# Kernel optimization log

Measured on AMD Instinct MI355X. Metric: run time of the kernel, lower is better.

Reference implementation:

```python
import jax, jax.numpy as jnp
import numpy as np

B, S, D_IN, D_QK, D_V = 4, 4096, 1024, 64, 64

def setup_inputs() -> dict:
    key = jax.random.key(0)
    ks = jax.random.split(key, 8)
    sd = 1.0 / np.sqrt(D_IN)
    return {
        "X": jax.random.normal(ks[0], (B, S, D_IN), dtype=jnp.float32),
        "mask": jnp.ones((B, S, 1), dtype=jnp.float32),
        "Wq": jax.random.uniform(ks[1], (D_IN, D_QK), jnp.float32, -sd, sd),
        "bq": jax.random.uniform(ks[2], (D_QK,), jnp.float32, -sd, sd),
        "Wk": jax.random.uniform(ks[3], (D_IN, D_QK), jnp.float32, -sd, sd),
        "bk": jax.random.uniform(ks[4], (D_QK,), jnp.float32, -sd, sd),
        "Wv": jax.random.uniform(ks[5], (D_IN, D_V), jnp.float32, -sd, sd),
        "bv": jax.random.uniform(ks[6], (D_V,), jnp.float32, -sd, sd),
    }

def reference(X, mask, Wq, bq, Wk, bk, Wv, bv):
    # ReLU-activated projections (no head split, no 1/sqrt(d) scaling)
    q = jax.nn.relu(jnp.einsum('bsd,df->bsf', X, Wq) + bq)   # [B,S,D_QK]
    k = jax.nn.relu(jnp.einsum('bsd,df->bsf', X, Wk) + bk)   # [B,S,D_QK]
    v = jax.nn.relu(jnp.einsum('bsd,df->bsf', X, Wv) + bv)   # [B,S,D_V]
    scores = jax.nn.softmax(jnp.einsum('bqf,bkf->bqk', q, k), axis=-1)  # [B,S,S]
    return jnp.einsum('bqk,bkf->bqf', scores, v) * mask       # mask applied AFTER AV
```

## Files before the change

kernel.cpp:

```cpp
#include <hip/hip_runtime.h>


typedef short s16x8 __attribute__((ext_vector_type(8)));
typedef float fx4   __attribute__((ext_vector_type(4)));
typedef unsigned short u16x4 __attribute__((ext_vector_type(4)));

#define LOG2E 1.4426950408889634f

__device__ __forceinline__ unsigned short f2bf(float x) {
    unsigned int u = __float_as_uint(x);
    u += 0x7FFFu + ((u >> 16) & 1u);
    return (unsigned short)(u >> 16);
}
__device__ __forceinline__ float bf2f(unsigned short b) {
    return __uint_as_float(((unsigned int)b) << 16);
}

__global__ __launch_bounds__(256) void prep_w_kernel(
    const float* __restrict__ Wq, const float* __restrict__ Wk, const float* __restrict__ Wv,
    unsigned short* __restrict__ wt_hi, unsigned short* __restrict__ wt_lo)
{
    __shared__ __align__(16) unsigned short sh[64][72];
    __shared__ __align__(16) unsigned short sl[64][72];

    const int y  = blockIdx.x;
    const int kt = blockIdx.y;
    const float* W = (y == 0) ? Wq : (y == 1) ? Wk : Wv;
    const int t  = threadIdx.x;

    const int kl = t >> 2;
    const int c0 = (t & 3) * 16;
    const float* src = W + (size_t)(kt * 64 + kl) * 64 + c0;
    #pragma unroll
    for (int j = 0; j < 4; j++) {
        fx4 v = *(const fx4*)(src + j * 4);
        #pragma unroll
        for (int i = 0; i < 4; i++) {
            float x = v[i];
            unsigned short h = f2bf(x);
            unsigned short l = f2bf(x - bf2f(h));
            sh[c0 + j * 4 + i][kl] = h;
            sl[c0 + j * 4 + i][kl] = l;
        }
    }
    __syncthreads();

    const int c  = t >> 2;
    const int k0 = (t & 3) * 16;
    size_t o = (size_t)(y * 64 + c) * 1024 + kt * 64 + k0;
    *(s16x8*)(wt_hi + o)     = *(const s16x8*)&sh[c][k0];
    *(s16x8*)(wt_hi + o + 8) = *(const s16x8*)&sh[c][k0 + 8];
    *(s16x8*)(wt_lo + o)     = *(const s16x8*)&sl[c][k0];
    *(s16x8*)(wt_lo + o + 8) = *(const s16x8*)&sl[c][k0 + 8];
}

__global__ __launch_bounds__(512, 4) void proj_kernel(
    const float* __restrict__ X,
    const unsigned short* __restrict__ wt_hi, const unsigned short* __restrict__ wt_lo,
    const float* __restrict__ bq, const float* __restrict__ bk, const float* __restrict__ bv,
    unsigned short* __restrict__ q_hi, unsigned short* __restrict__ q_lo,
    unsigned short* __restrict__ k_bf, unsigned short* __restrict__ vt_g)
{
    __shared__ __align__(16) unsigned short a_buf[2][64][72];
    __shared__ __align__(16) unsigned short b_hi[64][72];
    __shared__ __align__(16) unsigned short b_lo[64][72];

    const int tid  = threadIdx.x;
    const int lane = tid & 63;
    const int w    = tid >> 6;
    const int quad = lane >> 4;
    const int l15  = lane & 15;
    const int rs   = w & 3;
    const int ch   = w >> 2;

    const int f   = blockIdx.x;
    const int xcd = f & 7;
    const int jj  = f >> 3;
    const int y   = jj % 3;
    const int m0  = ((jj / 3) * 8 + xcd) * 64;

    fx4 acc[2];
    acc[0] = (fx4){0.f, 0.f, 0.f, 0.f};
    acc[1] = (fx4){0.f, 0.f, 0.f, 0.f};

    const int xrow = tid >> 4;
    const int xoff = (tid & 15) * 4;
    const int wrow = tid >> 3;
    const int woff = (tid & 7) * 8;

    const float* xb0 = X + (size_t)(m0 + xrow) * 1024 + xoff;
    const float* xb1 = X + (size_t)(m0 + xrow + 32) * 1024 + xoff;
    const size_t wb  = (size_t)(y * 64 + wrow) * 1024 + woff;

    fx4   xr[4][2];
    s16x8 wrh[2], wrl[2];
    #pragma unroll
    for (int d = 0; d < 4; d++) {
        xr[d][0] = *(const fx4*)(xb0 + d * 64);
        xr[d][1] = *(const fx4*)(xb1 + d * 64);
    }
    #pragma unroll
    for (int d = 0; d < 2; d++) {
        wrh[d] = *(const s16x8*)(wt_hi + wb + d * 64);
        wrl[d] = *(const s16x8*)(wt_lo + wb + d * 64);
    }

    #pragma unroll 4
    for (int kc = 0; kc < 16; kc++) {
        if (kc) __syncthreads();
        #pragma unroll
        for (int i = 0; i < 2; i++) {
            fx4 xv = xr[kc & 3][i];
            unsigned short h0 = f2bf(xv.x), h1 = f2bf(xv.y), h2 = f2bf(xv.z), h3 = f2bf(xv.w);
            unsigned short l0 = f2bf(xv.x - bf2f(h0)), l1 = f2bf(xv.y - bf2f(h1));
            unsigned short l2 = f2bf(xv.z - bf2f(h2)), l3 = f2bf(xv.w - bf2f(h3));
            *(u16x4*)&a_buf[0][xrow + i * 32][xoff] = (u16x4){h0, h1, h2, h3};
            *(u16x4*)&a_buf[1][xrow + i * 32][xoff] = (u16x4){l0, l1, l2, l3};
        }
        *(s16x8*)&b_hi[wrow][woff] = wrh[kc & 1];
        *(s16x8*)&b_lo[wrow][woff] = wrl[kc & 1];
        __syncthreads();

        if (kc < 12) {
            xr[kc & 3][0] = *(const fx4*)(xb0 + (kc + 4) * 64);
            xr[kc & 3][1] = *(const fx4*)(xb1 + (kc + 4) * 64);
        }
        if (kc < 14) {
            wrh[kc & 1] = *(const s16x8*)(wt_hi + wb + (kc + 2) * 64);
            wrl[kc & 1] = *(const s16x8*)(wt_lo + wb + (kc + 2) * 64);
        }

        s16x8 ah[2], al[2];
        #pragma unroll
        for (int ks = 0; ks < 2; ks++) {
            int r = rs * 16 + l15;
            ah[ks] = *(const s16x8*)&a_buf[0][r][ks * 32 + quad * 8];
            al[ks] = *(const s16x8*)&a_buf[1][r][ks * 32 + quad * 8];
        }
        #pragma unroll
        for (int nt = 0; nt < 2; nt++) {
            #pragma unroll
            for (int ks = 0; ks < 2; ks++) {
                s16x8 bh = *(const s16x8*)&b_hi[ch * 32 + nt * 16 + l15][ks * 32 + quad * 8];
                s16x8 bl = *(const s16x8*)&b_lo[ch * 32 + nt * 16 + l15][ks * 32 + quad * 8];
                acc[nt] = __builtin_amdgcn_mfma_f32_16x16x32_bf16(ah[ks], bh, acc[nt], 0, 0, 0);
                acc[nt] = __builtin_amdgcn_mfma_f32_16x16x32_bf16(ah[ks], bl, acc[nt], 0, 0, 0);
                acc[nt] = __builtin_amdgcn_mfma_f32_16x16x32_bf16(al[ks], bh, acc[nt], 0, 0, 0);
            }
        }
    }
    __syncthreads();

    const float* bias = (y == 0) ? bq : (y == 1) ? bk : bv;
    const int b   = m0 >> 12;
    const int s0b = m0 & 4095;
    unsigned short* vtr = &a_buf[0][0][0];

    #pragma unroll
    for (int nt = 0; nt < 2; nt++) {
        int col = ch * 32 + nt * 16 + l15;
        float bb = bias[col];
        int rloc = rs * 16 + quad * 4;
        #pragma unroll
        for (int r = 0; r < 4; r++) {
            float v = acc[nt][r] + bb;
            v = fmaxf(v, 0.f);
            size_t grow = (size_t)(m0 + rloc + r);
            if (y == 0) {
                unsigned short h = f2bf(v);
                unsigned short l = f2bf(v - bf2f(h));
                q_hi[grow * 64 + col] = h;
                q_lo[grow * 64 + col] = l;
            } else if (y == 1) {
                k_bf[grow * 64 + col] = f2bf(v);
            } else {
                vtr[col * 72 + rloc + r] = f2bf(v);
            }
        }
    }
    if (y == 2) {
        __syncthreads();
        int row = tid >> 3;
        int off = (tid & 7) * 8;
        s16x8 vv = *(const s16x8*)&vtr[row * 72 + off];
        *(s16x8*)(vt_g + (size_t)(b * 64 + row) * 4096 + s0b + off) = vv;
    }
}

__global__ __launch_bounds__(256, 6) void attn_kernel(
    const unsigned short* __restrict__ q_hi, const unsigned short* __restrict__ q_lo,
    const unsigned short* __restrict__ k_bf, const unsigned short* __restrict__ vt_g,
    unsigned short* __restrict__ pOb, float* __restrict__ pL)
{
    __shared__ __align__(16) unsigned short kt[64][72];
    __shared__ __align__(16) unsigned short vt[64][72];
    __shared__ __align__(16) unsigned short pt[4][16][40];

    const int tid  = threadIdx.x;
    const int lane = tid & 63;
    const int w    = tid >> 6;
    const int quad = lane >> 4;
    const int l15  = lane & 15;
    const int ck   = blockIdx.y;
    const int b    = blockIdx.z;
    const int q0   = blockIdx.x * 64;

    const size_t qoff = ((size_t)b * 4096 + q0 + w * 16 + l15) * 64 + quad * 8;
    s16x8 qh0 = *(const s16x8*)(q_hi + qoff);
    s16x8 qh1 = *(const s16x8*)(q_hi + qoff + 32);
    s16x8 ql0 = *(const s16x8*)(q_lo + qoff);
    s16x8 ql1 = *(const s16x8*)(q_lo + qoff + 32);

    fx4 accO[4];
    #pragma unroll
    for (int nt = 0; nt < 4; nt++) accO[nt] = (fx4){0.f, 0.f, 0.f, 0.f};
    float lsum[4] = {0.f, 0.f, 0.f, 0.f};

    const unsigned short* kgb = k_bf + (size_t)b * 4096 * 64;
    const unsigned short* vgb = vt_g + (size_t)b * 64 * 4096;

    const int srow = tid >> 3;
    const int soff = (tid & 7) * 8;

    for (int it = ck * 8; it < ck * 8 + 8; it++) {
        const unsigned short* kg = kgb + (size_t)it * 4096;
        #pragma unroll
        for (int i = 0; i < 2; i++) {
            int row = srow + i * 32;
            *(s16x8*)&kt[row][soff] = *(const s16x8*)(kg + (size_t)row * 64 + soff);
            *(s16x8*)&vt[row][soff] = *(const s16x8*)(vgb + (size_t)row * 4096 + it * 64 + soff);
        }
        __syncthreads();

        #pragma unroll
        for (int kh = 0; kh < 2; kh++) {
            #pragma unroll
            for (int nt2 = 0; nt2 < 2; nt2++) {
                int key = kh * 32 + nt2 * 16 + l15;
                s16x8 k0 = *(const s16x8*)&kt[key][quad * 8];
                s16x8 k1 = *(const s16x8*)&kt[key][32 + quad * 8];
                fx4 sc = (fx4){0.f, 0.f, 0.f, 0.f};
                sc = __builtin_amdgcn_mfma_f32_16x16x32_bf16(qh0, k0, sc, 0, 0, 0);
                sc = __builtin_amdgcn_mfma_f32_16x16x32_bf16(ql0, k0, sc, 0, 0, 0);
                sc = __builtin_amdgcn_mfma_f32_16x16x32_bf16(qh1, k1, sc, 0, 0, 0);
                sc = __builtin_amdgcn_mfma_f32_16x16x32_bf16(ql1, k1, sc, 0, 0, 0);
                #pragma unroll
                for (int r = 0; r < 4; r++) {
                    float p = __builtin_amdgcn_exp2f(sc[r] * LOG2E);
                    unsigned short pb = f2bf(p);
                    lsum[r] += bf2f(pb);
                    pt[w][quad * 4 + r][nt2 * 16 + l15] = pb;
                }
            }
            s16x8 pa = *(const s16x8*)&pt[w][l15][quad * 8];
            #pragma unroll
            for (int nt = 0; nt < 4; nt++) {
                s16x8 vf = *(const s16x8*)&vt[nt * 16 + l15][kh * 32 + quad * 8];
                accO[nt] = __builtin_amdgcn_mfma_f32_16x16x32_bf16(pa, vf, accO[nt], 0, 0, 0);
            }
        }
        __syncthreads();
    }

    #pragma unroll
    for (int r = 0; r < 4; r++) {
        float v = lsum[r];
        #pragma unroll
        for (int o = 1; o < 16; o <<= 1) v += __shfl_xor(v, o);
        lsum[r] = v;
    }
    #pragma unroll
    for (int r = 0; r < 4; r++) {
        int qrow = q0 + w * 16 + quad * 4 + r;
        size_t grow = (size_t)b * 4096 + qrow;
        #pragma unroll
        for (int nt = 0; nt < 4; nt++)
            pOb[((size_t)ck * 16384 + grow) * 64 + nt * 16 + l15] = f2bf(accO[nt][r]);
        if (l15 == 0)
            pL[(size_t)ck * 16384 + grow] = lsum[r];
    }
}

__global__ __launch_bounds__(256) void combine_kernel(
    const unsigned short* __restrict__ pOb, const float* __restrict__ pL,
    const float* __restrict__ mask, float* __restrict__ out)
{
    int idx = blockIdx.x * 256 + threadIdx.x;
    int q  = idx >> 4;
    int dg = idx & 15;
    fx4 s = (fx4){0.f, 0.f, 0.f, 0.f};
    float l = 0.f;
    #pragma unroll
    for (int c = 0; c < 8; c++) {
        u16x4 h = *(const u16x4*)(pOb + ((size_t)c * 16384 + q) * 64 + dg * 4);
        s.x += bf2f(h.x);
        s.y += bf2f(h.y);
        s.z += bf2f(h.z);
        s.w += bf2f(h.w);
        l += pL[(size_t)c * 16384 + q];
    }
    float scale = mask[q] / l;
    *(fx4*)(out + (size_t)q * 64 + dg * 4) = s * scale;
}

extern "C" void kernel_launch(void* const* d_in, const int* in_sizes, int n_in,
                              void* d_out, int out_size, void* d_ws, size_t ws_size,
                              hipStream_t stream)
{
    const float* X    = (const float*)d_in[0];
    const float* mask = (const float*)d_in[1];
    const float* Wq   = (const float*)d_in[2];
    const float* bq   = (const float*)d_in[3];
    const float* Wk   = (const float*)d_in[4];
    const float* bk   = (const float*)d_in[5];
    const float* Wv   = (const float*)d_in[6];
    const float* bv   = (const float*)d_in[7];
    float* out = (float*)d_out;

    char* ws = (char*)d_ws;
    unsigned short* q_hi  = (unsigned short*)(ws);
    unsigned short* q_lo  = (unsigned short*)(ws + (size_t)(2u << 20));
    unsigned short* k_bf  = (unsigned short*)(ws + (size_t)(4u << 20));
    unsigned short* vt_g  = (unsigned short*)(ws + (size_t)(6u << 20));
    unsigned short* wt_hi = (unsigned short*)(ws + (size_t)(8u << 20));
    unsigned short* wt_lo = (unsigned short*)(ws + (size_t)(8u << 20) + 393216);
    unsigned short* pOb   = (unsigned short*)(ws + (size_t)(9u << 20));
    float*          pL    = (float*)(ws + (size_t)(25u << 20));

    hipLaunchKernelGGL(prep_w_kernel, dim3(3, 16), dim3(256), 0, stream,
                       Wq, Wk, Wv, wt_hi, wt_lo);
    hipLaunchKernelGGL(proj_kernel, dim3(768), dim3(512), 0, stream,
                       X, wt_hi, wt_lo, bq, bk, bv, q_hi, q_lo, k_bf, vt_g);
    hipLaunchKernelGGL(attn_kernel, dim3(64, 8, 4), dim3(256), 0, stream,
                       q_hi, q_lo, k_bf, vt_g, pOb, pL);
    hipLaunchKernelGGL(combine_kernel, dim3(1024), dim3(256), 0, stream,
                       pOb, pL, mask, out);
}
```

Measured before the change: 179.1 us.

## Double-buffer X tiles in LDS and read weight fragments directly from global

The projection kernel now double-buffers the converted X hi/lo tiles in shared memory, so each k-step needs one barrier instead of two. Weight B-fragments are loaded straight from global/L2 into registers in MFMA layout rather than staged through LDS. The launch-bounds occupancy hint rises from 4 to 6. This cuts LDS traffic and syncs, at the cost of more global loads for weights (possibly redundant across waves) and more register pressure from the full unroll.

```diff
diff --git a/kernel.cpp b/kernel.cpp
--- a/kernel.cpp
+++ b/kernel.cpp
@@ -54,16 +54,14 @@
     *(s16x8*)(wt_lo + o + 8) = *(const s16x8*)&sl[c][k0 + 8];
 }
 
-__global__ __launch_bounds__(512, 4) void proj_kernel(
+__global__ __launch_bounds__(512, 6) void proj_kernel(
     const float* __restrict__ X,
     const unsigned short* __restrict__ wt_hi, const unsigned short* __restrict__ wt_lo,
     const float* __restrict__ bq, const float* __restrict__ bk, const float* __restrict__ bv,
     unsigned short* __restrict__ q_hi, unsigned short* __restrict__ q_lo,
     unsigned short* __restrict__ k_bf, unsigned short* __restrict__ vt_g)
 {
-    __shared__ __align__(16) unsigned short a_buf[2][64][72];
-    __shared__ __align__(16) unsigned short b_hi[64][72];
-    __shared__ __align__(16) unsigned short b_lo[64][72];
+    __shared__ __align__(16) unsigned short a_buf[2][2][64][72];
 
     const int tid  = threadIdx.x;
     const int lane = tid & 63;
@@ -85,76 +83,73 @@
 
     const int xrow = tid >> 4;
     const int xoff = (tid & 15) * 4;
-    const int wrow = tid >> 3;
-    const int woff = (tid & 7) * 8;
 
     const float* xb0 = X + (size_t)(m0 + xrow) * 1024 + xoff;
     const float* xb1 = X + (size_t)(m0 + xrow + 32) * 1024 + xoff;
-    const size_t wb  = (size_t)(y * 64 + wrow) * 1024 + woff;
-
-    fx4   xr[4][2];
-    s16x8 wrh[2], wrl[2];
-    #pragma unroll
-    for (int d = 0; d < 4; d++) {
-        xr[d][0] = *(const fx4*)(xb0 + d * 64);
-        xr[d][1] = *(const fx4*)(xb1 + d * 64);
-    }
-    #pragma unroll
-    for (int d = 0; d < 2; d++) {
-        wrh[d] = *(const s16x8*)(wt_hi + wb + d * 64);
-        wrl[d] = *(const s16x8*)(wt_lo + wb + d * 64);
-    }
-
-    #pragma unroll 4
-    for (int kc = 0; kc < 16; kc++) {
-        if (kc) __syncthreads();
+
+    const size_t wb = (size_t)(y * 64 + ch * 32 + l15) * 1024 + quad * 8;
+    const unsigned short* wph0 = wt_hi + wb;
+    const unsigned short* wph1 = wph0 + 16 * 1024;
+    const unsigned short* wpl0 = wt_lo + wb;
+    const unsigned short* wpl1 = wpl0 + 16 * 1024;
+
+    const int arow = rs * 16 + l15;
+    const int acol = quad * 8;
+
+    auto cvt_store = [&](int d, fx4 va, fx4 vb) {
         #pragma unroll
         for (int i = 0; i < 2; i++) {
-            fx4 xv = xr[kc & 3][i];
+            fx4 xv = i ? vb : va;
             unsigned short h0 = f2bf(xv.x), h1 = f2bf(xv.y), h2 = f2bf(xv.z), h3 = f2bf(xv.w);
             unsigned short l0 = f2bf(xv.x - bf2f(h0)), l1 = f2bf(xv.y - bf2f(h1));
             unsigned short l2 = f2bf(xv.z - bf2f(h2)), l3 = f2bf(xv.w - bf2f(h3));
-            *(u16x4*)&a_buf[0][xrow + i * 32][xoff] = (u16x4){h0, h1, h2, h3};
-            *(u16x4*)&a_buf[1][xrow + i * 32][xoff] = (u16x4){l0, l1, l2, l3};
-        }
-        *(s16x8*)&b_hi[wrow][woff] = wrh[kc & 1];
-        *(s16x8*)&b_lo[wrow][woff] = wrl[kc & 1];
-        __syncthreads();
-
-        if (kc < 12) {
-            xr[kc & 3][0] = *(const fx4*)(xb0 + (kc + 4) * 64);
-            xr[kc & 3][1] = *(const fx4*)(xb1 + (kc + 4) * 64);
-        }
-        if (kc < 14) {
-            wrh[kc & 1] = *(const s16x8*)(wt_hi + wb + (kc + 2) * 64);
-            wrl[kc & 1] = *(const s16x8*)(wt_lo + wb + (kc + 2) * 64);
-        }
-
+            *(u16x4*)&a_buf[d][0][xrow + i * 32][xoff] = (u16x4){h0, h1, h2, h3};
+            *(u16x4*)&a_buf[d][1][xrow + i * 32][xoff] = (u16x4){l0, l1, l2, l3};
+        }
+    };
+
+    fx4 xr[2][2];
+    cvt_store(0, *(const fx4*)(xb0), *(const fx4*)(xb1));
+    xr[1][0] = *(const fx4*)(xb0 + 64);
+    xr[1][1] = *(const fx4*)(xb1 + 64);
+    xr[0][0] = *(const fx4*)(xb0 + 128);
+    xr[0][1] = *(const fx4*)(xb1 + 128);
+    __syncthreads();
+
+    #pragma unroll
+    for (int kc = 0; kc < 16; kc++) {
+        const int cur = kc & 1;
+        if (kc < 15) cvt_store(cur ^ 1, xr[(kc + 1) & 1][0], xr[(kc + 1) & 1][1]);
+        if (kc < 13) {
+            xr[(kc + 1) & 1][0] = *(const fx4*)(xb0 + (kc + 3) * 64);
+            xr[(kc + 1) & 1][1] = *(const fx4*)(xb1 + (kc + 3) * 64);
+        }
         s16x8 ah[2], al[2];
         #pragma unroll
         for (int ks = 0; ks < 2; ks++) {
-            int r = rs * 16 + l15;
-            ah[ks] = *(const s16x8*)&a_buf[0][r][ks * 32 + quad * 8];
-            al[ks] = *(const s16x8*)&a_buf[1][r][ks * 32 + quad * 8];
+            ah[ks] = *(const s16x8*)&a_buf[cur][0][arow][ks * 32 + acol];
+            al[ks] = *(const s16x8*)&a_buf[cur][1][arow][ks * 32 + acol];
         }
         #pragma unroll
         for (int nt = 0; nt < 2; nt++) {
+            const unsigned short* ph = nt ? wph1 : wph0;
+            const unsigned short* pl = nt ? wpl1 : wpl0;
             #pragma unroll
             for (int ks = 0; ks < 2; ks++) {
-                s16x8 bh = *(const s16x8*)&b_hi[ch * 32 + nt * 16 + l15][ks * 32 + quad * 8];
-                s16x8 bl = *(const s16x8*)&b_lo[ch * 32 + nt * 16 + l15][ks * 32 + quad * 8];
+                s16x8 bh = *(const s16x8*)(ph + kc * 64 + ks * 32);
+                s16x8 bl = *(const s16x8*)(pl + kc * 64 + ks * 32);
                 acc[nt] = __builtin_amdgcn_mfma_f32_16x16x32_bf16(ah[ks], bh, acc[nt], 0, 0, 0);
                 acc[nt] = __builtin_amdgcn_mfma_f32_16x16x32_bf16(ah[ks], bl, acc[nt], 0, 0, 0);
                 acc[nt] = __builtin_amdgcn_mfma_f32_16x16x32_bf16(al[ks], bh, acc[nt], 0, 0, 0);
             }
         }
-    }
-    __syncthreads();
+        __syncthreads();
+    }
 
     const float* bias = (y == 0) ? bq : (y == 1) ? bk : bv;
     const int b   = m0 >> 12;
     const int s0b = m0 & 4095;
-    unsigned short* vtr = &a_buf[0][0][0];
+    unsigned short* vtr = &a_buf[0][0][0][0];
 
     #pragma unroll
     for (int nt = 0; nt < 2; nt++) {
```

New measurement: 230.2 us. 1.28x slower.
